# Performance work log

Measured on AMD Instinct MI355X. Metric: run time of the kernel, lower is better.

Reference implementation:

```python
import jax, jax.numpy as jnp
import numpy as np

N, E, F_IN, H_MID, D_OUT = 20000, 320000, 1024, 256, 128
SCALE_PARAM = 3.0
LEAKY_SLOPE = 0.01


def setup_inputs() -> dict:
    key = jax.random.key(0)
    ks = jax.random.split(key, 12)
    inv = lambda k, i, o: jax.random.normal(k, (i, o), jnp.float32) / np.sqrt(i)
    return {
        "x": jax.random.normal(ks[0], (N, F_IN), jnp.float32),
        "edge_index": jax.random.randint(ks[1], (2, E), 0, N, dtype=jnp.int64),
        "W_gcn": inv(ks[2], F_IN, H_MID),
        "b_gcn": jnp.zeros((H_MID,), jnp.float32),
        "Wq": inv(ks[3], H_MID, D_OUT), "bq": jnp.zeros((D_OUT,), jnp.float32),
        "Wk": inv(ks[4], H_MID, D_OUT), "bk": jnp.zeros((D_OUT,), jnp.float32),
        "Wv": inv(ks[5], H_MID, D_OUT), "bv": jnp.zeros((D_OUT,), jnp.float32),
        "Ws": inv(ks[6], H_MID, D_OUT), "bs": jnp.zeros((D_OUT,), jnp.float32),
    }


def reference(x, edge_index, W_gcn, b_gcn, Wq, bq, Wk, bk, Wv, bv, Ws, bs):
    n = x.shape[0]
    src, dst = edge_index[0], edge_index[1]  # message flows src(j) -> dst(i)

    # ---- GCNConv(feature_dim -> inter_dim), add_self_loops=True, sym norm ----
    loop = jnp.arange(n, dtype=src.dtype)
    row = jnp.concatenate([src, loop])
    col = jnp.concatenate([dst, loop])
    deg = jax.ops.segment_sum(jnp.ones(row.shape, x.dtype), col, num_segments=n)
    dinv = jnp.where(deg > 0, jax.lax.rsqrt(deg), 0.0)
    norm = dinv[row] * dinv[col]                      # [E+N]
    h = x @ W_gcn                                     # [N, H_MID]
    h = jax.ops.segment_sum(h[row] * norm[:, None], col, num_segments=n) + b_gcn
    h = jnp.where(h >= 0, h, LEAKY_SLOPE * h)         # LeakyReLU
    # Dropout(p) is identity at inference.

    # ---- TransformerConvReducrLayer (heads=1, no self loops, sigmoid score) ----
    d = Wq.shape[1]
    q = h @ Wq + bq
    k = h @ Wk + bk
    v = h @ Wv + bv
    alpha = jnp.sum(q[dst] * k[src], axis=-1) / jnp.sqrt(jnp.asarray(d, h.dtype))  # [E]
    alpha = alpha - alpha.mean()
    alpha = alpha / ((1.0 / SCALE_PARAM) * jnp.std(alpha, ddof=1))  # torch unbiased std
    alpha = jax.nn.sigmoid(alpha)
    msg = v[src] * alpha[:, None]                     # [E, D_OUT]
    out = jax.ops.segment_sum(msg, dst, num_segments=n)
    out = out + (h @ Ws + bs)                         # root_weight skip (PyG default)
    return out
```

## Files before the change

kernel.cpp:

```cpp
#include <hip/hip_runtime.h>
#include <hip/hip_bf16.h>

#define NNODES 20000
#define EEDGES 320000
#define FIN 1024
#define HMID 256
#define DOUT 128
#define ALPHA_BLOCKS ((NNODES + 3) / 4)

typedef __bf16 bf16x8 __attribute__((ext_vector_type(8)));
typedef __bf16 bf16x4 __attribute__((ext_vector_type(4)));
typedef __bf16 bf16x2 __attribute__((ext_vector_type(2)));
typedef float f32x4 __attribute__((ext_vector_type(4)));

typedef const __attribute__((address_space(1))) void* gas_ptr;
typedef __attribute__((address_space(3))) void* las_ptr;
__device__ __forceinline__ void async_copy16(const void* g, void* l) {
    __builtin_amdgcn_global_load_lds((gas_ptr)g, (las_ptr)l, 16, 0, 0);
}

__global__ void k_pack_w(const float* __restrict__ W, __bf16* __restrict__ Wtp) {
    int tid = blockIdx.x * 256 + threadIdx.x;
    int kk = tid >> 10;
    int rem = tid & 1023;
    int h = rem >> 9;
    int u = rem & 511;
    int kq = u >> 7, c = u & 127;
    int col = h * 128 + c;
    int k0 = kk * 32 + kq * 8;
    bf16x8 v;
#pragma unroll
    for (int j = 0; j < 8; j++)
        v[j] = (__bf16)W[(size_t)(k0 + j) * HMID + col];
    *(bf16x8*)(Wtp + (size_t)tid * 8) = v;
}

__global__ void k_prep_watt(const float* __restrict__ Wq, const float* __restrict__ Wk,
                            const float* __restrict__ Wv, const float* __restrict__ Ws,
                            const float* __restrict__ bq, const float* __restrict__ bk,
                            const float* __restrict__ bv, const float* __restrict__ bs,
                            __bf16* __restrict__ Wallt, float* __restrict__ ball) {
    int g = blockIdx.y;
    const float* W = (g == 0) ? Wq : (g == 1) ? Wk : (g == 2) ? Wv : Ws;
    int tid = blockIdx.x * 256 + threadIdx.x;
    int n = tid & 127;
    int k0u = tid >> 7;
    if (k0u < 32) {
        bf16x8 v;
#pragma unroll
        for (int j = 0; j < 8; j++)
            v[j] = (__bf16)W[(size_t)(k0u * 8 + j) * DOUT + n];
        *(bf16x8*)(Wallt + (size_t)(g * DOUT + n) * HMID + k0u * 8) = v;
    }
    if (tid < DOUT) {
        const float* b = (g == 0) ? bq : (g == 1) ? bk : (g == 2) ? bv : bs;
        ball[g * DOUT + tid] = b[tid];
    }
}

__global__ void k_init(int* __restrict__ cnt, float* __restrict__ S) {
    int i = blockIdx.x * 256 + threadIdx.x;
    if (i < NNODES) cnt[i] = 0;
    if (i < 16) S[i] = 0.0f;
}

__global__ void k_count(const int* __restrict__ dst, int* __restrict__ cnt) {
    int e = blockIdx.x * 256 + threadIdx.x;
    if (e < EEDGES) atomicAdd(&cnt[dst[e]], 1);
}

__global__ void k_dinv(const int* __restrict__ cnt, float* __restrict__ dinv,
                       int* __restrict__ cursor) {
    int i = blockIdx.x * 256 + threadIdx.x;
    if (i < NNODES) {
        dinv[i] = rsqrtf((float)cnt[i] + 1.0f);
        cursor[i] = 0;
    }
}

__global__ __launch_bounds__(1024) void k_scan(const int* __restrict__ cnt,
                                               int* __restrict__ rowptr) {
    __shared__ int sh[1024];
    int t = threadIdx.x;
    int base = t * 20;
    int local[20];
    int sum = 0;
#pragma unroll
    for (int j = 0; j < 20; j++) {
        int i = base + j;
        int v = (i < NNODES) ? cnt[i] : 0;
        local[j] = sum;
        sum += v;
    }
    sh[t] = sum;
    __syncthreads();
    for (int off = 1; off < 1024; off <<= 1) {
        int v = (t >= off) ? sh[t - off] : 0;
        __syncthreads();
        sh[t] += v;
        __syncthreads();
    }
    int prev = (t > 0) ? sh[t - 1] : 0;
#pragma unroll
    for (int j = 0; j < 20; j++) {
        int i = base + j;
        if (i < NNODES) rowptr[i] = prev + local[j];
    }
    if (t == 1023) rowptr[NNODES] = sh[1023];
}

__global__ void k_fill(const int* __restrict__ src, const int* __restrict__ dst,
                       const int* __restrict__ rowptr, int* __restrict__ cursor,
                       const float* __restrict__ dinv,
                       int* __restrict__ srcsorted, float* __restrict__ wsorted) {
    int e = blockIdx.x * 256 + threadIdx.x;
    if (e >= EEDGES) return;
    int d = dst[e];
    int s = src[e];
    int pos = atomicAdd(&cursor[d], 1);
    int w = rowptr[d] + pos;
    srcsorted[w] = s;
    wsorted[w] = dinv[s];
}

__global__ __launch_bounds__(256) void k_gemm1(const float* __restrict__ x,
                                               const __bf16* __restrict__ Wtp,
                                               __bf16* __restrict__ h0bf) {
    __shared__ __bf16 As[1024];
    __shared__ __bf16 Bs[4096];
    int t = threadIdx.x;
    int lane = t & 63;
    int m = lane & 15, q = lane >> 4;
    int w = t >> 6;
    int wc = w * 32;
    int r0 = blockIdx.x * 32;
    int h = blockIdx.y;
    int c0 = h * 128;

    int arow = t >> 3;
    const float* ap = x + (size_t)(r0 + arow) * FIN + (t & 7) * 4;
    __bf16* awr = &As[arow * 32 + ((t & 7) >> 1) * 8 + (t & 1) * 4];
    const __bf16* bb = Wtp + (size_t)h * 4096;

    f32x4 acc[2][2] = {};

    float4 a = *(const float4*)(ap);

#pragma unroll 1
    for (int kk = 0; kk < 32; kk++) {
        async_copy16(bb + (size_t)kk * 8192 + t * 8, &Bs[t * 8]);
        async_copy16(bb + (size_t)kk * 8192 + (t + 256) * 8, &Bs[(t + 256) * 8]);
        bf16x4 av;
        av[0] = (__bf16)a.x; av[1] = (__bf16)a.y; av[2] = (__bf16)a.z; av[3] = (__bf16)a.w;
        *(bf16x4*)awr = av;
        if (kk + 1 < 32) a = *(const float4*)(ap + (kk + 1) * 32);
        __syncthreads();

        bf16x8 af[2], bfr[2];
#pragma unroll
        for (int i = 0; i < 2; i++)
            af[i] = *(const bf16x8*)&As[(i * 16 + m) * 32 + q * 8];
#pragma unroll
        for (int jb = 0; jb < 2; jb++)
            bfr[jb] = *(const bf16x8*)&Bs[(q * 128 + wc + jb * 16 + m) * 8];
#pragma unroll
        for (int i = 0; i < 2; i++)
#pragma unroll
            for (int jb = 0; jb < 2; jb++)
                acc[i][jb] = __builtin_amdgcn_mfma_f32_16x16x32_bf16(af[i], bfr[jb], acc[i][jb], 0, 0, 0);
        __syncthreads();
    }

#pragma unroll
    for (int i = 0; i < 2; i++)
#pragma unroll
        for (int jb = 0; jb < 2; jb++)
#pragma unroll
            for (int r = 0; r < 4; r++) {
                int row = r0 + i * 16 + q * 4 + r;
                int col = c0 + wc + jb * 16 + m;
                h0bf[(size_t)row * 256 + col] = (__bf16)acc[i][jb][r];
            }
}

__global__ __launch_bounds__(256) void k_gcn_gather(const int* __restrict__ rowptr,
                                                    const int* __restrict__ srcsorted,
                                                    const float* __restrict__ wsorted,
                                                    const __bf16* __restrict__ h0bf,
                                                    const float* __restrict__ dinv,
                                                    const float* __restrict__ bgcn,
                                                    __bf16* __restrict__ hbf) {
    int gid = blockIdx.x * 256 + threadIdx.x;
    int n = gid >> 6, l = gid & 63;
    if (n >= NNODES) return;
    float dn = dinv[n];
    float wn = dn * dn;
    bf16x4 hv = *(const bf16x4*)(h0bf + (size_t)n * 256 + l * 4);
    float4 b = ((const float4*)bgcn)[l];
    float ax = (float)hv[0] * wn + b.x;
    float ay = (float)hv[1] * wn + b.y;
    float az = (float)hv[2] * wn + b.z;
    float aw = (float)hv[3] * wn + b.w;
    int beg = rowptr[n], end = rowptr[n + 1];
    for (int i = beg; i < end; i += 4) {
        int i1 = i + 1 < end ? i + 1 : end - 1;
        int i2 = i + 2 < end ? i + 2 : end - 1;
        int i3 = i + 3 < end ? i + 3 : end - 1;
        int s0 = srcsorted[i], s1 = srcsorted[i1], s2 = srcsorted[i2], s3 = srcsorted[i3];
        float w0 = wsorted[i] * dn;
        float w1 = (i + 1 < end) ? wsorted[i1] * dn : 0.f;
        float w2 = (i + 2 < end) ? wsorted[i2] * dn : 0.f;
        float w3 = (i + 3 < end) ? wsorted[i3] * dn : 0.f;
        bf16x4 v0 = *(const bf16x4*)(h0bf + (size_t)s0 * 256 + l * 4);
        bf16x4 v1 = *(const bf16x4*)(h0bf + (size_t)s1 * 256 + l * 4);
        bf16x4 v2 = *(const bf16x4*)(h0bf + (size_t)s2 * 256 + l * 4);
        bf16x4 v3 = *(const bf16x4*)(h0bf + (size_t)s3 * 256 + l * 4);
        ax += (float)v0[0] * w0 + (float)v1[0] * w1 + (float)v2[0] * w2 + (float)v3[0] * w3;
        ay += (float)v0[1] * w0 + (float)v1[1] * w1 + (float)v2[1] * w2 + (float)v3[1] * w3;
        az += (float)v0[2] * w0 + (float)v1[2] * w1 + (float)v2[2] * w2 + (float)v3[2] * w3;
        aw += (float)v0[3] * w0 + (float)v1[3] * w1 + (float)v2[3] * w2 + (float)v3[3] * w3;
    }
    bf16x4 o;
    o[0] = (__bf16)(ax >= 0.f ? ax : 0.01f * ax);
    o[1] = (__bf16)(ay >= 0.f ? ay : 0.01f * ay);
    o[2] = (__bf16)(az >= 0.f ? az : 0.01f * az);
    o[3] = (__bf16)(aw >= 0.f ? aw : 0.01f * aw);
    *(bf16x4*)(hbf + (size_t)n * 256 + l * 4) = o;
}

__global__ __launch_bounds__(256) void k_gemm2(const __bf16* __restrict__ hbf,
                                               const __bf16* __restrict__ Wallt,
                                               const float* __restrict__ ball,
                                               __bf16* __restrict__ qarr,
                                               __bf16* __restrict__ karr,
                                               __bf16* __restrict__ varr,
                                               __bf16* __restrict__ sarr) {
    __shared__ __bf16 As[4096];
    __shared__ __bf16 Bs[4096];
    int t = threadIdx.x;
    int lane = t & 63;
    int m = lane & 15, q = lane >> 4;
    int wave = t >> 6;
    int wr = (wave & 1) * 64;
    int wc = (wave >> 1) * 64;
    int r0 = blockIdx.x * 128;
    int c0 = blockIdx.y * 128;
    __bf16* tbl = (blockIdx.y == 0) ? qarr : (blockIdx.y == 1) ? karr
                : (blockIdx.y == 2) ? varr : sarr;

    const __bf16* asrc[2];
    __bf16* aldst[2];
#pragma unroll
    for (int j = 0; j < 2; j++) {
        int u = j * 256 + t;
        int row = r0 + (u & 127);
        if (row >= NNODES) row = NNODES - 1;
        asrc[j] = hbf + (size_t)row * HMID + (u >> 7) * 8;
        aldst[j] = &As[(size_t)u * 8];
    }
    const __bf16* bsrc[2];
    __bf16* bldst[2];
#pragma unroll
    for (int j = 0; j < 2; j++) {
        int u = j * 256 + t;
        bsrc[j] = Wallt + (size_t)(c0 + (u & 127)) * HMID + (u >> 7) * 8;
        bldst[j] = &Bs[(size_t)u * 8];
    }

    f32x4 acc[4][4] = {};

    for (int k0 = 0; k0 < HMID; k0 += 32) {
#pragma unroll
        for (int j = 0; j < 2; j++) async_copy16(asrc[j] + k0, aldst[j]);
#pragma unroll
        for (int j = 0; j < 2; j++) async_copy16(bsrc[j] + k0, bldst[j]);
        __syncthreads();

        bf16x8 af[4], bfr[4];
#pragma unroll
        for (int i = 0; i < 4; i++) af[i] = *(const bf16x8*)&As[(size_t)(q * 128 + wr + i * 16 + m) * 8];
#pragma unroll
        for (int jb = 0; jb < 4; jb++) bfr[jb] = *(const bf16x8*)&Bs[(size_t)(q * 128 + wc + jb * 16 + m) * 8];
#pragma unroll
        for (int i = 0; i < 4; i++)
#pragma unroll
            for (int jb = 0; jb < 4; jb++)
                acc[i][jb] = __builtin_amdgcn_mfma_f32_16x16x32_bf16(af[i], bfr[jb], acc[i][jb], 0, 0, 0);
        __syncthreads();
    }

#pragma unroll
    for (int jb = 0; jb < 4; jb++) {
        int dcol = wc + jb * 16 + m;
        float bias = ball[c0 + dcol];
#pragma unroll
        for (int i = 0; i < 4; i++)
#pragma unroll
            for (int r = 0; r < 4; r++) {
                int row = r0 + wr + i * 16 + q * 4 + r;
                if (row < NNODES) tbl[(size_t)row * 128 + dcol] = (__bf16)(acc[i][jb][r] + bias);
            }
    }
}

__global__ __launch_bounds__(256) void k_alpha(const int* __restrict__ rowptr,
                                               const int* __restrict__ srcsorted,
                                               const __bf16* __restrict__ qarr,
                                               const __bf16* __restrict__ karr,
                                               float* __restrict__ alpha,
                                               float* __restrict__ part) {
    int n = (blockIdx.x * 256 + threadIdx.x) >> 6;
    int lane = threadIdx.x & 63;
    int g = lane >> 4, l = lane & 15;
    float s1 = 0.f, s2 = 0.f;
    if (n < NNODES) {
        bf16x8 qb = *(const bf16x8*)(qarr + (size_t)n * 128 + l * 8);
        float qf[8];
#pragma unroll
        for (int j = 0; j < 8; j++) qf[j] = (float)qb[j];
        int beg = rowptr[n], end = rowptr[n + 1];
        for (int i = beg + g; i < end; i += 16) {
            int i1 = i + 4 < end ? i + 4 : end - 1;
            int i2 = i + 8 < end ? i + 8 : end - 1;
            int i3 = i + 12 < end ? i + 12 : end - 1;
            int s0 = srcsorted[i], sA = srcsorted[i1], sB = srcsorted[i2], sC = srcsorted[i3];
            bf16x8 k0 = *(const bf16x8*)(karr + (size_t)s0 * 128 + l * 8);
            bf16x8 k1 = *(const bf16x8*)(karr + (size_t)sA * 128 + l * 8);
            bf16x8 k2 = *(const bf16x8*)(karr + (size_t)sB * 128 + l * 8);
            bf16x8 k3 = *(const bf16x8*)(karr + (size_t)sC * 128 + l * 8);
            float d0 = 0.f, d1 = 0.f, d2 = 0.f, d3 = 0.f;
#pragma unroll
            for (int j = 0; j < 8; j++) {
                d0 += qf[j] * (float)k0[j];
                d1 += qf[j] * (float)k1[j];
                d2 += qf[j] * (float)k2[j];
                d3 += qf[j] * (float)k3[j];
            }
#pragma unroll
            for (int off = 1; off < 16; off <<= 1) {
                d0 += __shfl_xor(d0, off, 64);
                d1 += __shfl_xor(d1, off, 64);
                d2 += __shfl_xor(d2, off, 64);
                d3 += __shfl_xor(d3, off, 64);
            }
            if (l == 0) {
                const float sc = 0.08838834764831845f;
                float a0 = d0 * sc;
                alpha[i] = a0; s1 += a0; s2 += a0 * a0;
                if (i + 4 < end)  { float a = d1 * sc; alpha[i + 4]  = a; s1 += a; s2 += a * a; }
                if (i + 8 < end)  { float a = d2 * sc; alpha[i + 8]  = a; s1 += a; s2 += a * a; }
                if (i + 12 < end) { float a = d3 * sc; alpha[i + 12] = a; s1 += a; s2 += a * a; }
            }
        }
    }
#pragma unroll
    for (int off = 1; off < 64; off <<= 1) {
        s1 += __shfl_xor(s1, off, 64);
        s2 += __shfl_xor(s2, off, 64);
    }
    __shared__ float sh[8];
    int wave = threadIdx.x >> 6;
    if ((threadIdx.x & 63) == 0) { sh[wave] = s1; sh[4 + wave] = s2; }
    __syncthreads();
    if (threadIdx.x == 0) {
        part[2 * blockIdx.x]     = sh[0] + sh[1] + sh[2] + sh[3];
        part[2 * blockIdx.x + 1] = sh[4] + sh[5] + sh[6] + sh[7];
    }
}

__global__ __launch_bounds__(1024) void k_stats(const float* __restrict__ part,
                                                float* __restrict__ S) {
    float s1 = 0.f, s2 = 0.f;
    for (int i = threadIdx.x; i < ALPHA_BLOCKS; i += 1024) {
        s1 += part[2 * i];
        s2 += part[2 * i + 1];
    }
#pragma unroll
    for (int off = 1; off < 64; off <<= 1) {
        s1 += __shfl_xor(s1, off, 64);
        s2 += __shfl_xor(s2, off, 64);
    }
    __shared__ float sh1[16], sh2[16];
    int wave = threadIdx.x >> 6;
    if ((threadIdx.x & 63) == 0) { sh1[wave] = s1; sh2[wave] = s2; }
    __syncthreads();
    if (threadIdx.x == 0) {
        float t1 = 0.f, t2 = 0.f;
#pragma unroll
        for (int w = 0; w < 16; w++) { t1 += sh1[w]; t2 += sh2[w]; }
        float mean = t1 / (float)EEDGES;
        float var = (t2 - (float)EEDGES * mean * mean) / (float)(EEDGES - 1);
        float stdv = sqrtf(fmaxf(var, 1e-20f));
        S[2] = mean;
        S[3] = 3.0f / stdv;
    }
}

__global__ __launch_bounds__(256) void k_msg_gather(const int* __restrict__ rowptr,
                                                    const int* __restrict__ srcsorted,
                                                    const __bf16* __restrict__ varr,
                                                    const __bf16* __restrict__ sarr,
                                                    const float* __restrict__ alpha,
                                                    const float* __restrict__ S,
                                                    float* __restrict__ out) {
    int n = (blockIdx.x * 256 + threadIdx.x) >> 6;
    int l = threadIdx.x & 63;
    if (n >= NNODES) return;
    float mean = S[2], scl = S[3];
    bf16x2 sb = *(const bf16x2*)(sarr + (size_t)n * 128 + l * 2);
    float ax = (float)sb[0], ay = (float)sb[1];
    int beg = rowptr[n], end = rowptr[n + 1];
    for (int i = beg; i < end; i += 4) {
        int i1 = i + 1 < end ? i + 1 : end - 1;
        int i2 = i + 2 < end ? i + 2 : end - 1;
        int i3 = i + 3 < end ? i + 3 : end - 1;
        int s0 = srcsorted[i], s1 = srcsorted[i1], s2 = srcsorted[i2], s3 = srcsorted[i3];
        float z0 = (alpha[i] - mean) * scl;
        float z1 = (alpha[i1] - mean) * scl;
        float z2 = (alpha[i2] - mean) * scl;
        float z3 = (alpha[i3] - mean) * scl;
        float g0 = 1.0f / (1.0f + __expf(-z0));
        float g1 = (i + 1 < end) ? 1.0f / (1.0f + __expf(-z1)) : 0.f;
        float g2 = (i + 2 < end) ? 1.0f / (1.0f + __expf(-z2)) : 0.f;
        float g3 = (i + 3 < end) ? 1.0f / (1.0f + __expf(-z3)) : 0.f;
        bf16x2 v0 = *(const bf16x2*)(varr + (size_t)s0 * 128 + l * 2);
        bf16x2 v1 = *(const bf16x2*)(varr + (size_t)s1 * 128 + l * 2);
        bf16x2 v2 = *(const bf16x2*)(varr + (size_t)s2 * 128 + l * 2);
        bf16x2 v3 = *(const bf16x2*)(varr + (size_t)s3 * 128 + l * 2);
        ax += (float)v0[0] * g0 + (float)v1[0] * g1 + (float)v2[0] * g2 + (float)v3[0] * g3;
        ay += (float)v0[1] * g0 + (float)v1[1] * g1 + (float)v2[1] * g2 + (float)v3[1] * g3;
    }
    float2 o; o.x = ax; o.y = ay;
    ((float2*)(out + (size_t)n * DOUT))[l] = o;
}

extern "C" void kernel_launch(void* const* d_in, const int* in_sizes, int n_in,
                              void* d_out, int out_size, void* d_ws, size_t ws_size,
                              hipStream_t stream) {
    const float* x  = (const float*)d_in[0];
    const int* ei   = (const int*)d_in[1];
    const int* srcI = ei;
    const int* dstI = ei + EEDGES;
    const float* Wg = (const float*)d_in[2];
    const float* bg = (const float*)d_in[3];
    const float* Wq = (const float*)d_in[4];  const float* bq = (const float*)d_in[5];
    const float* Wk = (const float*)d_in[6];  const float* bk = (const float*)d_in[7];
    const float* Wv = (const float*)d_in[8];  const float* bv = (const float*)d_in[9];
    const float* Ws = (const float*)d_in[10]; const float* bs = (const float*)d_in[11];
    float* out = (float*)d_out;

    char* wsb = (char*)d_ws;
    size_t off = 0;
    auto alloc = [&](size_t bytes) -> void* {
        void* p = wsb + off;
        off += (bytes + 255) & ~(size_t)255;
        return p;
    };
    int*    cnt    = (int*)alloc((size_t)NNODES * 4);
    int*    rowptr = (int*)alloc((size_t)(NNODES + 1) * 4);
    int*    cursor = (int*)alloc((size_t)NNODES * 4);
    int*    srcst  = (int*)alloc((size_t)EEDGES * 4);
    float*  wsort  = (float*)alloc((size_t)EEDGES * 4);
    float*  dinv   = (float*)alloc((size_t)NNODES * 4);
    float*  S      = (float*)alloc(64);
    float*  part   = (float*)alloc((size_t)ALPHA_BLOCKS * 2 * 4);
    __bf16* Wtp    = (__bf16*)alloc((size_t)32 * 8192 * 2);
    __bf16* Wallt  = (__bf16*)alloc((size_t)512 * HMID * 2);
    float*  ball   = (float*)alloc(512 * 4);
    __bf16* h0bf   = (__bf16*)alloc((size_t)NNODES * HMID * 2);
    __bf16* hbf    = (__bf16*)alloc((size_t)NNODES * HMID * 2);
    __bf16* qarr   = (__bf16*)alloc((size_t)NNODES * 128 * 2);
    __bf16* karr   = (__bf16*)alloc((size_t)NNODES * 128 * 2);
    __bf16* varr   = (__bf16*)alloc((size_t)NNODES * 128 * 2);
    __bf16* sarr   = (__bf16*)alloc((size_t)NNODES * 128 * 2);
    float*  alphab = (float*)alloc((size_t)EEDGES * 4);
    if (off > ws_size) return;

    k_pack_w<<<128, 256, 0, stream>>>(Wg, Wtp);
    dim3 gw(16, 4);
    k_prep_watt<<<gw, 256, 0, stream>>>(Wq, Wk, Wv, Ws, bq, bk, bv, bs, Wallt, ball);

    k_init<<<(NNODES + 255) / 256, 256, 0, stream>>>(cnt, S);
    k_count<<<(EEDGES + 255) / 256, 256, 0, stream>>>(dstI, cnt);
    k_dinv<<<(NNODES + 255) / 256, 256, 0, stream>>>(cnt, dinv, cursor);
    k_scan<<<1, 1024, 0, stream>>>(cnt, rowptr);
    k_fill<<<(EEDGES + 255) / 256, 256, 0, stream>>>(srcI, dstI, rowptr, cursor, dinv, srcst, wsort);

    dim3 g1(625, 2);
    k_gemm1<<<g1, 256, 0, stream>>>(x, Wtp, h0bf);

    k_gcn_gather<<<(NNODES * 64 + 255) / 256, 256, 0, stream>>>(rowptr, srcst, wsort, h0bf, dinv, bg, hbf);

    dim3 g2((NNODES + 127) / 128, 4);
    k_gemm2<<<g2, 256, 0, stream>>>(hbf, Wallt, ball, qarr, karr, varr, sarr);

    k_alpha<<<ALPHA_BLOCKS, 256, 0, stream>>>(rowptr, srcst, qarr, karr, alphab, part);
    k_stats<<<1, 1024, 0, stream>>>(part, S);

    k_msg_gather<<<(NNODES * 64 + 255) / 256, 256, 0, stream>>>(rowptr, srcst, varr, sarr, alphab, S, out);
}
```

Baseline: 315.9 us.

## Load edge lists once per wave and broadcast via readlane; shrink gemm2 row tile

In the GCN and message gather kernels, each lane now loads one edge's source index and weight (or sigmoid gate) cooperatively, then the wave broadcasts them with readlane instead of every lane redundantly loading the same index/weight per edge. Edges beyond 64 fall back to a serial loop. This removes redundant scalar-per-lane loads and redundant sigmoid evaluation, at the cost of serial readlane iteration. Separately, gemm2 uses a 64-row tile instead of 128 to double the block count for better occupancy across CUs.

```diff
diff --git a/kernel.cpp b/kernel.cpp
--- a/kernel.cpp
+++ b/kernel.cpp
@@ -17,6 +17,10 @@
 typedef __attribute__((address_space(3))) void* las_ptr;
 __device__ __forceinline__ void async_copy16(const void* g, void* l) {
     __builtin_amdgcn_global_load_lds((gas_ptr)g, (las_ptr)l, 16, 0, 0);
+}
+
+__device__ __forceinline__ float readlane_f(float v, int lane) {
+    return __uint_as_float(__builtin_amdgcn_readlane(__float_as_uint(v), lane));
 }
 
 __global__ void k_pack_w(const float* __restrict__ W, __bf16* __restrict__ Wtp) {
@@ -202,23 +206,37 @@
     float az = (float)hv[2] * wn + b.z;
     float aw = (float)hv[3] * wn + b.w;
     int beg = rowptr[n], end = rowptr[n + 1];
-    for (int i = beg; i < end; i += 4) {
-        int i1 = i + 1 < end ? i + 1 : end - 1;
-        int i2 = i + 2 < end ? i + 2 : end - 1;
-        int i3 = i + 3 < end ? i + 3 : end - 1;
-        int s0 = srcsorted[i], s1 = srcsorted[i1], s2 = srcsorted[i2], s3 = srcsorted[i3];
-        float w0 = wsorted[i] * dn;
-        float w1 = (i + 1 < end) ? wsorted[i1] * dn : 0.f;
-        float w2 = (i + 2 < end) ? wsorted[i2] * dn : 0.f;
-        float w3 = (i + 3 < end) ? wsorted[i3] * dn : 0.f;
-        bf16x4 v0 = *(const bf16x4*)(h0bf + (size_t)s0 * 256 + l * 4);
-        bf16x4 v1 = *(const bf16x4*)(h0bf + (size_t)s1 * 256 + l * 4);
-        bf16x4 v2 = *(const bf16x4*)(h0bf + (size_t)s2 * 256 + l * 4);
-        bf16x4 v3 = *(const bf16x4*)(h0bf + (size_t)s3 * 256 + l * 4);
-        ax += (float)v0[0] * w0 + (float)v1[0] * w1 + (float)v2[0] * w2 + (float)v3[0] * w3;
-        ay += (float)v0[1] * w0 + (float)v1[1] * w1 + (float)v2[1] * w2 + (float)v3[1] * w3;
-        az += (float)v0[2] * w0 + (float)v1[2] * w1 + (float)v2[2] * w2 + (float)v3[2] * w3;
-        aw += (float)v0[3] * w0 + (float)v1[3] * w1 + (float)v2[3] * w2 + (float)v3[3] * w3;
+    int deg = end - beg;
+    int degc = deg < 64 ? deg : 64;
+
+    int sidx = 0; float swt = 0.f;
+    if (l < degc) {
+        sidx = srcsorted[beg + l];
+        swt = wsorted[beg + l] * dn;
+    }
+
+    for (int e0 = 0; e0 < degc; e0 += 8) {
+#pragma unroll
+        for (int j = 0; j < 8; j++) {
+            int e = e0 + j;
+            if (e >= degc) break;
+            int s = __builtin_amdgcn_readlane(sidx, e);
+            float wv = readlane_f(swt, e);
+            bf16x4 v = *(const bf16x4*)(h0bf + (size_t)s * 256 + l * 4);
+            ax += (float)v[0] * wv;
+            ay += (float)v[1] * wv;
+            az += (float)v[2] * wv;
+            aw += (float)v[3] * wv;
+        }
+    }
+    for (int i = beg + 64; i < end; i++) {
+        int s = srcsorted[i];
+        float wv = wsorted[i] * dn;
+        bf16x4 v = *(const bf16x4*)(h0bf + (size_t)s * 256 + l * 4);
+        ax += (float)v[0] * wv;
+        ay += (float)v[1] * wv;
+        az += (float)v[2] * wv;
+        aw += (float)v[3] * wv;
     }
     bf16x4 o;
     o[0] = (__bf16)(ax >= 0.f ? ax : 0.01f * ax);
@@ -235,54 +253,46 @@
                                                __bf16* __restrict__ karr,
                                                __bf16* __restrict__ varr,
                                                __bf16* __restrict__ sarr) {
-    __shared__ __bf16 As[4096];
+    __shared__ __bf16 As[2048];
     __shared__ __bf16 Bs[4096];
     int t = threadIdx.x;
     int lane = t & 63;
     int m = lane & 15, q = lane >> 4;
     int wave = t >> 6;
-    int wr = (wave & 1) * 64;
+    int wr = (wave & 1) * 32;
     int wc = (wave >> 1) * 64;
-    int r0 = blockIdx.x * 128;
+    int r0 = blockIdx.x * 64;
     int c0 = blockIdx.y * 128;
     __bf16* tbl = (blockIdx.y == 0) ? qarr : (blockIdx.y == 1) ? karr
                 : (blockIdx.y == 2) ? varr : sarr;
 
-    const __bf16* asrc[2];
-    __bf16* aldst[2];
-#pragma unroll
-    for (int j = 0; j < 2; j++) {
-        int u = j * 256 + t;
-        int row = r0 + (u & 127);
-        if (row >= NNODES) row = NNODES - 1;
-        asrc[j] = hbf + (size_t)row * HMID + (u >> 7) * 8;
-        aldst[j] = &As[(size_t)u * 8];
-    }
-    const __bf16* bsrc[2];
-    __bf16* bldst[2];
-#pragma unroll
-    for (int j = 0; j < 2; j++) {
-        int u = j * 256 + t;
-        bsrc[j] = Wallt + (size_t)(c0 + (u & 127)) * HMID + (u >> 7) * 8;
-        bldst[j] = &Bs[(size_t)u * 8];
-    }
-
-    f32x4 acc[4][4] = {};
+    int arow = r0 + (t & 63);
+    if (arow >= NNODES) arow = NNODES - 1;
+    const __bf16* asrc = hbf + (size_t)arow * HMID + (t >> 6) * 8;
+    __bf16* aldst = &As[(size_t)t * 8];
+    int u1 = t + 256;
+    const __bf16* bsrc0 = Wallt + (size_t)(c0 + (t & 127)) * HMID + (t >> 7) * 8;
+    __bf16* bldst0 = &Bs[(size_t)t * 8];
+    const __bf16* bsrc1 = Wallt + (size_t)(c0 + (u1 & 127)) * HMID + (u1 >> 7) * 8;
+    __bf16* bldst1 = &Bs[(size_t)u1 * 8];
+
+    f32x4 acc[2][4] = {};
 
     for (int k0 = 0; k0 < HMID; k0 += 32) {
-#pragma unroll
-        for (int j = 0; j < 2; j++) async_copy16(asrc[j] + k0, aldst[j]);
-#pragma unroll
-        for (int j = 0; j < 2; j++) async_copy16(bsrc[j] + k0, bldst[j]);
+        async_copy16(asrc + k0, aldst);
+        async_copy16(bsrc0 + k0, bldst0);
+        async_copy16(bsrc1 + k0, bldst1);
         __syncthreads();
 
-        bf16x8 af[4], bfr[4];
-#pragma unroll
-        for (int i = 0; i < 4; i++) af[i] = *(const bf16x8*)&As[(size_t)(q * 128 + wr + i * 16 + m) * 8];
-#pragma unroll
-        for (int jb = 0; jb < 4; jb++) bfr[jb] = *(const bf16x8*)&Bs[(size_t)(q * 128 + wc + jb * 16 + m) * 8];
-#pragma unroll
-        for (int i = 0; i < 4; i++)
+        bf16x8 af[2], bfr[4];
+#pragma unroll
+        for (int i = 0; i < 2; i++)
+            af[i] = *(const bf16x8*)&As[(size_t)(q * 64 + wr + i * 16 + m) * 8];
+#pragma unroll
+        for (int jb = 0; jb < 4; jb++)
+            bfr[jb] = *(const bf16x8*)&Bs[(size_t)(q * 128 + wc + jb * 16 + m) * 8];
+#pragma unroll
+        for (int i = 0; i < 2; i++)
 #pragma unroll
             for (int jb = 0; jb < 4; jb++)
                 acc[i][jb] = __builtin_amdgcn_mfma_f32_16x16x32_bf16(af[i], bfr[jb], acc[i][jb], 0, 0, 0);
@@ -294,7 +304,7 @@
         int dcol = wc + jb * 16 + m;
         float bias = ball[c0 + dcol];
 #pragma unroll
-        for (int i = 0; i < 4; i++)
+        for (int i = 0; i < 2; i++)
 #pragma unroll
             for (int r = 0; r < 4; r++) {
                 int row = r0 + wr + i * 16 + q * 4 + r;
@@ -410,25 +420,35 @@
     bf16x2 sb = *(const bf16x2*)(sarr + (size_t)n * 128 + l * 2);
     float ax = (float)sb[0], ay = (float)sb[1];
     int beg = rowptr[n], end = rowptr[n + 1];
-    for (int i = beg; i < end; i += 4) {
-        int i1 = i + 1 < end ? i + 1 : end - 1;
-        int i2 = i + 2 < end ? i + 2 : end - 1;
-        int i3 = i + 3 < end ? i + 3 : end - 1;
-        int s0 = srcsorted[i], s1 = srcsorted[i1], s2 = srcsorted[i2], s3 = srcsorted[i3];
-        float z0 = (alpha[i] - mean) * scl;
-        float z1 = (alpha[i1] - mean) * scl;
-        float z2 = (alpha[i2] - mean) * scl;
-        float z3 = (alpha[i3] - mean) * scl;
-        float g0 = 1.0f / (1.0f + __expf(-z0));
-        float g1 = (i + 1 < end) ? 1.0f / (1.0f + __expf(-z1)) : 0.f;
-        float g2 = (i + 2 < end) ? 1.0f / (1.0f + __expf(-z2)) : 0.f;
-        float g3 = (i + 3 < end) ? 1.0f / (1.0f + __expf(-z3)) : 0.f;
-        bf16x2 v0 = *(const bf16x2*)(varr + (size_t)s0 * 128 + l * 2);
-        bf16x2 v1 = *(const bf16x2*)(varr + (size_t)s1 * 128 + l * 2);
-        bf16x2 v2 = *(const bf16x2*)(varr + (size_t)s2 * 128 + l * 2);
-        bf16x2 v3 = *(const bf16x2*)(varr + (size_t)s3 * 128 + l * 2);
-        ax += (float)v0[0] * g0 + (float)v1[0] * g1 + (float)v2[0] * g2 + (float)v3[0] * g3;
-        ay += (float)v0[1] * g0 + (float)v1[1] * g1 + (float)v2[1] * g2 + (float)v3[1] * g3;
+    int deg = end - beg;
+    int degc = deg < 64 ? deg : 64;
+
+    int sidx = 0; float gate = 0.f;
+    if (l < degc) {
+        sidx = srcsorted[beg + l];
+        float z = (alpha[beg + l] - mean) * scl;
+        gate = 1.0f / (1.0f + __expf(-z));
+    }
+
+    for (int e0 = 0; e0 < degc; e0 += 8) {
+#pragma unroll
+        for (int j = 0; j < 8; j++) {
+            int e = e0 + j;
+            if (e >= degc) break;
+            int s = __builtin_amdgcn_readlane(sidx, e);
+            float gv = readlane_f(gate, e);
+            bf16x2 v = *(const bf16x2*)(varr + (size_t)s * 128 + l * 2);
+            ax += (float)v[0] * gv;
+            ay += (float)v[1] * gv;
+        }
+    }
+    for (int i = beg + 64; i < end; i++) {
+        int s = srcsorted[i];
+        float z = (alpha[i] - mean) * scl;
+        float gv = 1.0f / (1.0f + __expf(-z));
+        bf16x2 v = *(const bf16x2*)(varr + (size_t)s * 128 + l * 2);
+        ax += (float)v[0] * gv;
+        ay += (float)v[1] * gv;
     }
     float2 o; o.x = ax; o.y = ay;
     ((float2*)(out + (size_t)n * DOUT))[l] = o;
@@ -491,7 +511,7 @@
 
     k_gcn_gather<<<(NNODES * 64 + 255) / 256, 256, 0, stream>>>(rowptr, srcst, wsort, h0bf, dinv, bg, hbf);
 
-    dim3 g2((NNODES + 127) / 128, 4);
+    dim3 g2(313, 4);
     k_gemm2<<<g2, 256, 0, stream>>>(hbf, Wallt, ball, qarr, karr, varr, sarr);
 
     k_alpha<<<ALPHA_BLOCKS, 256, 0, stream>>>(rowptr, srcst, qarr, karr, alphab, part);
```

Measured after the change: 314.5 us. About the same (-0.4%).
